# Performance work log

Measured on AMD Instinct MI355X. Metric: run time of the kernel, lower is better.

Reference implementation:

```python
import jax, jax.numpy as jnp
import numpy as np

IGNORE_INDEX = -100
BETA = 0.1
ALPHA = 1.0
LABEL_SMOOTHING = 0.0
GAMMA = 0.5

B, T, H, V = 8, 512, 2048, 32000


def setup_inputs() -> dict:
    key = jax.random.key(0)
    k1, k2, k3 = jax.random.split(key, 3)
    lin_weight = jax.random.normal(k1, (V, H), dtype=jnp.float32) * 0.02
    _input = jax.random.normal(k2, (B, T, H), dtype=jnp.float32)
    target = jax.random.randint(k3, (B, T), 0, V, dtype=jnp.int64)
    bias = jnp.zeros((V,), dtype=jnp.float32)
    return {"lin_weight": lin_weight, "_input": _input, "target": target, "bias": bias}


def reference(lin_weight, _input, target, bias):
    # Fused linear + SimPO preference loss (unfused jax reference).
    # _input: (B, T, H); first B/2 rows are 'chosen', last B/2 are 'rejected'.
    b = _input.shape[0]
    half = b // 2
    # logits: (B, T, V) -- the big tensor the Liger kernel avoids materializing
    logits = jnp.einsum("bth,vh->btv", _input, lin_weight) + bias
    log_probs = jax.nn.log_softmax(logits, axis=-1)
    # per-token log prob of the target token: (B, T)
    tok_logps = jnp.take_along_axis(log_probs, target[..., None], axis=-1)[..., 0]
    mask = (target != IGNORE_INDEX)
    maskf = mask.astype(tok_logps.dtype)
    # average log prob per sequence (SimPO length-normalization)
    avg_logps = (tok_logps * maskf).sum(-1) / maskf.sum(-1)
    chosen_logps = avg_logps[:half]
    rejected_logps = avg_logps[half:]
    # NLL loss on chosen half (compute_nll_loss=True), sum / num valid chosen tokens
    nll_loss = -(tok_logps[:half] * maskf[:half]).sum() / maskf[:half].sum()
    # SimPO sigmoid preference loss
    z = BETA * (chosen_logps - rejected_logps) - GAMMA
    pref_loss = (-jax.nn.log_sigmoid(z) * (1.0 - LABEL_SMOOTHING)
                 - jax.nn.log_sigmoid(-z) * LABEL_SMOOTHING).sum() / half
    loss = ALPHA * nll_loss + pref_loss
    return loss
```

## Files before the change

kernel.cpp:

```cpp
#include <hip/hip_runtime.h>
#include <hip/hip_bf16.h>


constexpr int Bb = 8, Tt = 512, Hh = 2048, Vv = 32000;
constexpr int Mrows = Bb * Tt;
constexpr int K4 = Hh / 4;
constexpr int BM = 128, BN = 128, BK = 64;
constexpr int NRT = Mrows / BM;
constexpr int NVT = Vv / BN;
constexpr int NVT2 = NVT * 2;
constexpr int NKS = Hh / BK;
constexpr int LDK = BK + 8;

typedef __attribute__((ext_vector_type(8))) short short8;
typedef __attribute__((ext_vector_type(4))) float f32x4;
typedef unsigned short ushort_t;

__device__ __forceinline__ unsigned pkbf2(float x, float y) {
  const unsigned ux = __builtin_bit_cast(unsigned, x);
  const unsigned uy = __builtin_bit_cast(unsigned, y);
  const unsigned rx = (ux + 0x7fffu + ((ux >> 16) & 1u)) >> 16;
  const unsigned ry = (uy + 0x7fffu + ((uy >> 16) & 1u)) >> 16;
  return (rx & 0xffffu) | (ry << 16);
}

__device__ __forceinline__ void gload16(const void* g, void* l) {
  __builtin_amdgcn_global_load_lds(
      (const __attribute__((address_space(1))) unsigned*)g,
      (__attribute__((address_space(3))) unsigned*)l, 16, 0, 0);
}

__global__ __launch_bounds__(256) void cvt_kernel(
    const float* __restrict__ src, unsigned* __restrict__ dst, int n4)
{
  const int stride = gridDim.x * 256;
  for (int i = blockIdx.x * 256 + threadIdx.x; i < n4; i += stride) {
    const float4 v = ((const float4*)src)[i];
    uint2 o;
    o.x = pkbf2(v.x, v.y);
    o.y = pkbf2(v.z, v.w);
    ((uint2*)dst)[i] = o;
  }
}

__device__ __forceinline__ void lse_epilogue(
    f32x4 (&acc)[4][4], const float* __restrict__ bias,
    float* __restrict__ pmax, float* __restrict__ psum,
    int rt, int vt, int wr, int wc, int lane)
{
  const int lane15 = lane & 15, q = lane >> 4;
  const int pcol = vt * 2 + (wc >> 6);
  float bj[4];
#pragma unroll
  for (int j = 0; j < 4; ++j) bj[j] = bias[vt * BN + wc + j * 16 + lane15];
#pragma unroll
  for (int i = 0; i < 4; ++i) {
#pragma unroll
    for (int r = 0; r < 4; ++r) {
      const float v0 = acc[i][0][r] + bj[0];
      const float v1 = acc[i][1][r] + bj[1];
      const float v2 = acc[i][2][r] + bj[2];
      const float v3 = acc[i][3][r] + bj[3];
      float mx = fmaxf(fmaxf(v0, v1), fmaxf(v2, v3));
#pragma unroll
      for (int m = 1; m < 16; m <<= 1) mx = fmaxf(mx, __shfl_xor(mx, m));
      float sm = __expf(v0 - mx) + __expf(v1 - mx) + __expf(v2 - mx) + __expf(v3 - mx);
#pragma unroll
      for (int m = 1; m < 16; m <<= 1) sm += __shfl_xor(sm, m);
      if (lane15 == 0) {
        const int grow = rt * BM + wr + i * 16 + q * 4 + r;
        pmax[(size_t)grow * NVT2 + pcol] = mx;
        psum[(size_t)grow * NVT2 + pcol] = sm;
      }
    }
  }
}

__global__ __launch_bounds__(256) void gemm_bf16(
    const ushort_t* __restrict__ Wb, const ushort_t* __restrict__ inpb,
    const float* __restrict__ bias,
    float* __restrict__ pmax, float* __restrict__ psum)
{
  __shared__ ushort_t At[BM][BK];
  __shared__ ushort_t Bt[BN][BK];

  const int tid = threadIdx.x;
  const int o  = (blockIdx.x & 7) * (NRT * NVT / 8) + (blockIdx.x >> 3);
  const int vt = o >> 5;
  const int rt = o & 31;

  const int lane = tid & 63;
  const int wv = tid >> 6;
  const int wr = (wv >> 1) * 64;
  const int wc = (wv & 1) * 64;

  const ushort_t* gA = inpb + (size_t)(rt * BM + wv * 32 + (lane >> 3)) * Hh + (lane & 7) * 8;
  const ushort_t* gB = Wb   + (size_t)(vt * BN + wv * 32 + (lane >> 3)) * Hh + (lane & 7) * 8;
  ushort_t* lA = &At[0][0] + wv * 2048 + lane * 8;
  ushort_t* lB = &Bt[0][0] + wv * 2048 + lane * 8;

  f32x4 acc[4][4];
#pragma unroll
  for (int i = 0; i < 4; ++i)
#pragma unroll
    for (int j = 0; j < 4; ++j) acc[i][j] = {0.f, 0.f, 0.f, 0.f};

  for (int ks = 0; ks < NKS; ++ks) {
#pragma unroll
    for (int c = 0; c < 4; ++c) {
      gload16(gA + (size_t)c * 8 * Hh + ks * BK, lA + c * 512);
      gload16(gB + (size_t)c * 8 * Hh + ks * BK, lB + c * 512);
    }
    __syncthreads();
#pragma unroll
    for (int kk = 0; kk < 2; ++kk) {
      const int kb = kk * 32 + (lane >> 4) * 8;
      const int rr = lane & 15;
      short8 a[4], b[4];
#pragma unroll
      for (int i = 0; i < 4; ++i) a[i] = *(const short8*)&At[wr + i * 16 + rr][kb];
#pragma unroll
      for (int j = 0; j < 4; ++j) b[j] = *(const short8*)&Bt[wc + j * 16 + rr][kb];
#pragma unroll
      for (int i = 0; i < 4; ++i)
#pragma unroll
        for (int j = 0; j < 4; ++j)
          acc[i][j] = __builtin_amdgcn_mfma_f32_16x16x32_bf16(a[i], b[j], acc[i][j], 0, 0, 0);
    }
    __syncthreads();
  }

  lse_epilogue(acc, bias, pmax, psum, rt, vt, wr, wc, lane);
}

__global__ __launch_bounds__(256) void gemm_partials(
    const float* __restrict__ W, const float* __restrict__ inp,
    const float* __restrict__ bias,
    float* __restrict__ pmax, float* __restrict__ psum)
{
  __shared__ ushort_t At[BM][LDK];
  __shared__ ushort_t Bt[BN][LDK];

  const int tid = threadIdx.x;
  const int o  = (blockIdx.x & 7) * (NRT * NVT / 8) + (blockIdx.x >> 3);
  const int vt = o >> 5;
  const int rt = o & 31;

  const int lane = tid & 63;
  const int wv = tid >> 6;
  const int wr = (wv >> 1) * 64;
  const int wc = (wv & 1) * 64;
  const int r0 = tid >> 4;
  const int c4 = tid & 15;

  const float4* Ag = (const float4*)inp + (size_t)(rt * BM) * K4;
  const float4* Bg = (const float4*)W  + (size_t)(vt * BN) * K4;

  float4 ar[8], br[8];
  auto issue = [&](int ks) {
    const int kb = ks * (BK / 4);
#pragma unroll
    for (int it = 0; it < 8; ++it) {
      ar[it] = Ag[(size_t)(r0 + it * 16) * K4 + kb + c4];
      br[it] = Bg[(size_t)(r0 + it * 16) * K4 + kb + c4];
    }
  };

  f32x4 acc[4][4];
#pragma unroll
  for (int i = 0; i < 4; ++i)
#pragma unroll
    for (int j = 0; j < 4; ++j) acc[i][j] = {0.f, 0.f, 0.f, 0.f};

  issue(0);
  for (int ks = 0; ks < NKS; ++ks) {
    __syncthreads();
#pragma unroll
    for (int it = 0; it < 8; ++it) {
      uint2 ua, ub;
      ua.x = pkbf2(ar[it].x, ar[it].y); ua.y = pkbf2(ar[it].z, ar[it].w);
      ub.x = pkbf2(br[it].x, br[it].y); ub.y = pkbf2(br[it].z, br[it].w);
      *(uint2*)&At[r0 + it * 16][c4 * 4] = ua;
      *(uint2*)&Bt[r0 + it * 16][c4 * 4] = ub;
    }
    __syncthreads();
    if (ks + 1 < NKS) issue(ks + 1);
#pragma unroll
    for (int kk = 0; kk < 2; ++kk) {
      const int kb = kk * 32 + (lane >> 4) * 8;
      const int rr = lane & 15;
      short8 a[4], b[4];
#pragma unroll
      for (int i = 0; i < 4; ++i) a[i] = *(const short8*)&At[wr + i * 16 + rr][kb];
#pragma unroll
      for (int j = 0; j < 4; ++j) b[j] = *(const short8*)&Bt[wc + j * 16 + rr][kb];
#pragma unroll
      for (int i = 0; i < 4; ++i)
#pragma unroll
        for (int j = 0; j < 4; ++j)
          acc[i][j] = __builtin_amdgcn_mfma_f32_16x16x32_bf16(a[i], b[j], acc[i][j], 0, 0, 0);
    }
  }

  lse_epilogue(acc, bias, pmax, psum, rt, vt, wr, wc, lane);
}

__global__ __launch_bounds__(256) void tgt_kernel(
    const float* __restrict__ inp, const float* __restrict__ W,
    const int* __restrict__ target, const float* __restrict__ bias,
    float* __restrict__ tl)
{
  const int row = blockIdx.x;
  int tgt = target[row];
  const int tgtc = tgt < 0 ? 0 : tgt;
  const float4* a = (const float4*)inp + (size_t)row * K4;
  const float4* w = (const float4*)W + (size_t)tgtc * K4;
  const int t = threadIdx.x;
  float s = 0.f;
  for (int i = t; i < K4; i += 256) {
    const float4 x = a[i], y = w[i];
    s += x.x * y.x + x.y * y.y + x.z * y.z + x.w * y.w;
  }
#pragma unroll
  for (int m = 1; m < 64; m <<= 1) s += __shfl_xor(s, m);
  __shared__ float red[4];
  if ((t & 63) == 0) red[t >> 6] = s;
  __syncthreads();
  if (t == 0) tl[row] = red[0] + red[1] + red[2] + red[3] + bias[tgtc];
}

__global__ __launch_bounds__(64) void lse_kernel(
    const float* __restrict__ pmax, const float* __restrict__ psum,
    const float* __restrict__ tl, float* __restrict__ tok)
{
  const int row = blockIdx.x;
  const int l = threadIdx.x;
  const float* pm = pmax + (size_t)row * NVT2;
  const float* ps = psum + (size_t)row * NVT2;
  float M = -3.4e38f;
  for (int t = l; t < NVT2; t += 64) M = fmaxf(M, pm[t]);
#pragma unroll
  for (int m = 1; m < 64; m <<= 1) M = fmaxf(M, __shfl_xor(M, m));
  float S = 0.f;
  for (int t = l; t < NVT2; t += 64) S += ps[t] * __expf(pm[t] - M);
#pragma unroll
  for (int m = 1; m < 64; m <<= 1) S += __shfl_xor(S, m);
  if (l == 0) tok[row] = tl[row] - (M + logf(S));
}

__global__ __launch_bounds__(512) void final_kernel(
    const float* __restrict__ tok, const int* __restrict__ target,
    float* __restrict__ out)
{
  const int w = threadIdx.x >> 6;
  const int l = threadIdx.x & 63;
  float s = 0.f, c = 0.f;
  for (int i = l; i < Tt; i += 64) {
    const int row = w * Tt + i;
    const bool msk = target[row] != -100;
    s += msk ? tok[row] : 0.f;
    c += msk ? 1.f : 0.f;
  }
#pragma unroll
  for (int m = 1; m < 64; m <<= 1) { s += __shfl_xor(s, m); c += __shfl_xor(c, m); }
  __shared__ float sums[8], cnts[8];
  if (l == 0) { sums[w] = s; cnts[w] = c; }
  __syncthreads();
  if (threadIdx.x == 0) {
    float avg[8];
    float nsum = 0.f, ncnt = 0.f;
    for (int b = 0; b < 8; ++b) {
      avg[b] = sums[b] / cnts[b];
      if (b < 4) { nsum += sums[b]; ncnt += cnts[b]; }
    }
    const float nll = -nsum / ncnt;
    float pref = 0.f;
    for (int i = 0; i < 4; ++i) {
      const float z = 0.1f * (avg[i] - avg[i + 4]) - 0.5f;
      const float ls = fminf(z, 0.f) - log1pf(__expf(-fabsf(z)));
      pref += -ls;
    }
    pref *= 0.25f;
    out[0] = 1.0f * nll + pref;
  }
}

extern "C" void kernel_launch(void* const* d_in, const int* in_sizes, int n_in,
                              void* d_out, int out_size, void* d_ws, size_t ws_size,
                              hipStream_t stream) {
  const float* W    = (const float*)d_in[0];
  const float* inp  = (const float*)d_in[1];
  const int*   tgt  = (const int*)d_in[2];
  const float* bias = (const float*)d_in[3];
  char* ws = (char*)d_ws;

  constexpr size_t szWb   = (size_t)Vv * Hh * 2;
  constexpr size_t szInb  = (size_t)Mrows * Hh * 2;
  constexpr size_t szPart = (size_t)Mrows * NVT2 * 4;
  constexpr size_t need   = szWb + szInb + 2 * szPart + 2 * (size_t)Mrows * 4;

  if (ws_size >= need) {
    ushort_t* Wb   = (ushort_t*)ws;
    ushort_t* inpb = (ushort_t*)(ws + szWb);
    float* pmax = (float*)(ws + szWb + szInb);
    float* psum = (float*)(ws + szWb + szInb + szPart);
    float* tl   = (float*)(ws + szWb + szInb + 2 * szPart);
    float* tok  = (float*)(ws + szWb + szInb + 2 * szPart + (size_t)Mrows * 4);

    hipLaunchKernelGGL(cvt_kernel, dim3(2048), dim3(256), 0, stream,
                       W, (unsigned*)Wb, Vv * Hh / 4);
    hipLaunchKernelGGL(cvt_kernel, dim3(2048), dim3(256), 0, stream,
                       inp, (unsigned*)inpb, Mrows * Hh / 4);
    hipLaunchKernelGGL(gemm_bf16, dim3(NRT * NVT), dim3(256), 0, stream,
                       Wb, inpb, bias, pmax, psum);
    hipLaunchKernelGGL(tgt_kernel, dim3(Mrows), dim3(256), 0, stream,
                       inp, W, tgt, bias, tl);
    hipLaunchKernelGGL(lse_kernel, dim3(Mrows), dim3(64), 0, stream,
                       pmax, psum, tl, tok);
    hipLaunchKernelGGL(final_kernel, dim3(1), dim3(512), 0, stream,
                       tok, tgt, (float*)d_out);
  } else {
    float* pmax = (float*)ws;
    float* psum = (float*)(ws + szPart);
    float* tl   = (float*)(ws + 2 * szPart);
    float* tok  = (float*)(ws + 2 * szPart + (size_t)Mrows * 4);

    hipLaunchKernelGGL(gemm_partials, dim3(NRT * NVT), dim3(256), 0, stream,
                       W, inp, bias, pmax, psum);
    hipLaunchKernelGGL(tgt_kernel, dim3(Mrows), dim3(256), 0, stream,
                       inp, W, tgt, bias, tl);
    hipLaunchKernelGGL(lse_kernel, dim3(Mrows), dim3(64), 0, stream,
                       pmax, psum, tl, tok);
    hipLaunchKernelGGL(final_kernel, dim3(1), dim3(512), 0, stream,
                       tok, tgt, (float*)d_out);
  }
}
```

Measured before the change: 1.135 ms.

## Replace bf16 GEMM with 256x256 tiled, double-buffered, swizzled LDS pipeline

```diff
diff --git a/kernel.cpp b/kernel.cpp
--- a/kernel.cpp
+++ b/kernel.cpp
@@ -5,12 +5,10 @@
 constexpr int Bb = 8, Tt = 512, Hh = 2048, Vv = 32000;
 constexpr int Mrows = Bb * Tt;
 constexpr int K4 = Hh / 4;
-constexpr int BM = 128, BN = 128, BK = 64;
-constexpr int NRT = Mrows / BM;
-constexpr int NVT = Vv / BN;
-constexpr int NVT2 = NVT * 2;
-constexpr int NKS = Hh / BK;
-constexpr int LDK = BK + 8;
+constexpr int NVT2 = Vv / 64;
+constexpr int NT64 = Hh / 64;
+constexpr int BMf = 128, BNf = 128, LDK = 64 + 8;
+constexpr int NRTf = Mrows / BMf, NVTf = Vv / BNf, NKSf = Hh / 64;
 
 typedef __attribute__((ext_vector_type(8))) short short8;
 typedef __attribute__((ext_vector_type(4))) float f32x4;
@@ -43,18 +41,128 @@
   }
 }
 
-__device__ __forceinline__ void lse_epilogue(
-    f32x4 (&acc)[4][4], const float* __restrict__ bias,
-    float* __restrict__ pmax, float* __restrict__ psum,
-    int rt, int vt, int wr, int wc, int lane)
-{
-  const int lane15 = lane & 15, q = lane >> 4;
-  const int pcol = vt * 2 + (wc >> 6);
+__global__ __launch_bounds__(512, 2) void gemm256(
+    const ushort_t* __restrict__ Wb, const ushort_t* __restrict__ inpb,
+    const float* __restrict__ bias,
+    float* __restrict__ pmax, float* __restrict__ psum)
+{
+  extern __shared__ ushort_t lds[];
+
+  const int tid = threadIdx.x;
+  const int l  = tid & 63;
+  const int wv = tid >> 6;
+  const int wm = wv >> 2;
+  const int wn = wv & 3;
+
+  const int o  = ((int)blockIdx.x & 7) * 250 + ((int)blockIdx.x >> 3);
+  const int bn = o >> 4;
+  const int bm = o & 15;
+  const int rowA0 = bm * 256, rowB0 = bn * 256;
+
+  const int segr = l >> 3;
+  const int csrc = (l & 7) ^ segr;
+  const int arow = l & 15;
+  const int kcb  = l >> 4;
+  const int sx   = l & 7;
+
+  auto stage = [&](int H) {
+    if (H >= 4 * NT64) return;
+    const int T = H >> 2, m = H & 3;
+    const ushort_t* src = (m < 2) ? inpb : Wb;
+    const int r0 = ((m < 2) ? rowA0 : rowB0) + (m & 1) * 128;
+    ushort_t* reg = lds + ((((T & 1) << 2) | m) << 13);
+    const int kc = T * 64 + csrc * 8;
+#pragma unroll
+    for (int s = 0; s < 2; ++s) {
+      const int seg = s * 8 + wv;
+      gload16(src + (size_t)(r0 + seg * 8 + segr) * Hh + kc,
+              reg + seg * 512 + l * 8);
+    }
+  };
+
+  f32x4 acc[8][4];
+#pragma unroll
+  for (int i = 0; i < 8; ++i)
+#pragma unroll
+    for (int j = 0; j < 4; ++j) acc[i][j] = {0.f, 0.f, 0.f, 0.f};
+
+#pragma unroll
+  for (int h = 0; h < 6; ++h) stage(h);
+  asm volatile("s_waitcnt vmcnt(4)" ::: "memory");
+  __builtin_amdgcn_s_barrier();
+
+  const int browbase = (wn & 1) * 64;
+  for (int t = 0; t < NT64; ++t) {
+    const int bA = ((((t & 1) << 2) | wm) << 13);
+    const int bB = ((((t & 1) << 2) | (2 + (wn >> 1))) << 13);
+    short8 a0[8], a1[8], b0[4], b1[4];
+
+#pragma unroll
+    for (int i = 0; i < 8; ++i)
+      a0[i] = *(const short8*)(lds + bA + (i * 16 + arow) * 64 + ((kcb ^ sx) * 8));
+#pragma unroll
+    for (int j = 0; j < 4; ++j)
+      b0[j] = *(const short8*)(lds + bB + (browbase + j * 16 + arow) * 64 + ((kcb ^ sx) * 8));
+    stage(4 * t + 6);
+    __builtin_amdgcn_s_barrier();
+    __builtin_amdgcn_s_setprio(1);
+#pragma unroll
+    for (int i = 0; i < 8; ++i)
+#pragma unroll
+      for (int j = 0; j < 2; ++j)
+        acc[i][j] = __builtin_amdgcn_mfma_f32_16x16x32_bf16(a0[i], b0[j], acc[i][j], 0, 0, 0);
+    __builtin_amdgcn_s_setprio(0);
+    __builtin_amdgcn_s_barrier();
+
+#pragma unroll
+    for (int i = 0; i < 8; ++i)
+      a1[i] = *(const short8*)(lds + bA + (i * 16 + arow) * 64 + (((4 + kcb) ^ sx) * 8));
+#pragma unroll
+    for (int j = 0; j < 4; ++j)
+      b1[j] = *(const short8*)(lds + bB + (browbase + j * 16 + arow) * 64 + (((4 + kcb) ^ sx) * 8));
+    stage(4 * t + 7);
+    __builtin_amdgcn_s_barrier();
+    __builtin_amdgcn_s_setprio(1);
+#pragma unroll
+    for (int i = 0; i < 8; ++i)
+#pragma unroll
+      for (int j = 2; j < 4; ++j)
+        acc[i][j] = __builtin_amdgcn_mfma_f32_16x16x32_bf16(a0[i], b0[j], acc[i][j], 0, 0, 0);
+    __builtin_amdgcn_s_setprio(0);
+    __builtin_amdgcn_s_barrier();
+
+    stage(4 * t + 8);
+    __builtin_amdgcn_s_barrier();
+    __builtin_amdgcn_s_setprio(1);
+#pragma unroll
+    for (int i = 0; i < 8; ++i)
+#pragma unroll
+      for (int j = 0; j < 2; ++j)
+        acc[i][j] = __builtin_amdgcn_mfma_f32_16x16x32_bf16(a1[i], b1[j], acc[i][j], 0, 0, 0);
+    __builtin_amdgcn_s_setprio(0);
+    __builtin_amdgcn_s_barrier();
+
+    stage(4 * t + 9);
+    __builtin_amdgcn_s_barrier();
+    __builtin_amdgcn_s_setprio(1);
+#pragma unroll
+    for (int i = 0; i < 8; ++i)
+#pragma unroll
+      for (int j = 2; j < 4; ++j)
+        acc[i][j] = __builtin_amdgcn_mfma_f32_16x16x32_bf16(a1[i], b1[j], acc[i][j], 0, 0, 0);
+    __builtin_amdgcn_s_setprio(0);
+    if (t < NT64 - 2)      asm volatile("s_waitcnt vmcnt(4)" ::: "memory");
+    else if (t == NT64 - 2) asm volatile("s_waitcnt vmcnt(0)" ::: "memory");
+    __builtin_amdgcn_s_barrier();
+  }
+
+  const int q = l >> 4;
+  const int pcol = bn * 4 + wn;
   float bj[4];
 #pragma unroll
-  for (int j = 0; j < 4; ++j) bj[j] = bias[vt * BN + wc + j * 16 + lane15];
-#pragma unroll
-  for (int i = 0; i < 4; ++i) {
+  for (int j = 0; j < 4; ++j) bj[j] = bias[bn * 256 + wn * 64 + j * 16 + arow];
+#pragma unroll
+  for (int i = 0; i < 8; ++i) {
 #pragma unroll
     for (int r = 0; r < 4; ++r) {
       const float v0 = acc[i][0][r] + bj[0];
@@ -67,70 +175,13 @@
       float sm = __expf(v0 - mx) + __expf(v1 - mx) + __expf(v2 - mx) + __expf(v3 - mx);
 #pragma unroll
       for (int m = 1; m < 16; m <<= 1) sm += __shfl_xor(sm, m);
-      if (lane15 == 0) {
-        const int grow = rt * BM + wr + i * 16 + q * 4 + r;
+      if (arow == 0) {
+        const int grow = bm * 256 + wm * 128 + i * 16 + q * 4 + r;
         pmax[(size_t)grow * NVT2 + pcol] = mx;
         psum[(size_t)grow * NVT2 + pcol] = sm;
       }
     }
   }
-}
-
-__global__ __launch_bounds__(256) void gemm_bf16(
-    const ushort_t* __restrict__ Wb, const ushort_t* __restrict__ inpb,
-    const float* __restrict__ bias,
-    float* __restrict__ pmax, float* __restrict__ psum)
-{
-  __shared__ ushort_t At[BM][BK];
-  __shared__ ushort_t Bt[BN][BK];
-
-  const int tid = threadIdx.x;
-  const int o  = (blockIdx.x & 7) * (NRT * NVT / 8) + (blockIdx.x >> 3);
-  const int vt = o >> 5;
-  const int rt = o & 31;
-
-  const int lane = tid & 63;
-  const int wv = tid >> 6;
-  const int wr = (wv >> 1) * 64;
-  const int wc = (wv & 1) * 64;
-
-  const ushort_t* gA = inpb + (size_t)(rt * BM + wv * 32 + (lane >> 3)) * Hh + (lane & 7) * 8;
-  const ushort_t* gB = Wb   + (size_t)(vt * BN + wv * 32 + (lane >> 3)) * Hh + (lane & 7) * 8;
-  ushort_t* lA = &At[0][0] + wv * 2048 + lane * 8;
-  ushort_t* lB = &Bt[0][0] + wv * 2048 + lane * 8;
-
-  f32x4 acc[4][4];
-#pragma unroll
-  for (int i = 0; i < 4; ++i)
-#pragma unroll
-    for (int j = 0; j < 4; ++j) acc[i][j] = {0.f, 0.f, 0.f, 0.f};
-
-  for (int ks = 0; ks < NKS; ++ks) {
-#pragma unroll
-    for (int c = 0; c < 4; ++c) {
-      gload16(gA + (size_t)c * 8 * Hh + ks * BK, lA + c * 512);
-      gload16(gB + (size_t)c * 8 * Hh + ks * BK, lB + c * 512);
-    }
-    __syncthreads();
-#pragma unroll
-    for (int kk = 0; kk < 2; ++kk) {
-      const int kb = kk * 32 + (lane >> 4) * 8;
-      const int rr = lane & 15;
-      short8 a[4], b[4];
-#pragma unroll
-      for (int i = 0; i < 4; ++i) a[i] = *(const short8*)&At[wr + i * 16 + rr][kb];
-#pragma unroll
-      for (int j = 0; j < 4; ++j) b[j] = *(const short8*)&Bt[wc + j * 16 + rr][kb];
-#pragma unroll
-      for (int i = 0; i < 4; ++i)
-#pragma unroll
-        for (int j = 0; j < 4; ++j)
-          acc[i][j] = __builtin_amdgcn_mfma_f32_16x16x32_bf16(a[i], b[j], acc[i][j], 0, 0, 0);
-    }
-    __syncthreads();
-  }
-
-  lse_epilogue(acc, bias, pmax, psum, rt, vt, wr, wc, lane);
 }
 
 __global__ __launch_bounds__(256) void gemm_partials(
@@ -138,11 +189,11 @@
     const float* __restrict__ bias,
     float* __restrict__ pmax, float* __restrict__ psum)
 {
-  __shared__ ushort_t At[BM][LDK];
-  __shared__ ushort_t Bt[BN][LDK];
+  __shared__ ushort_t At[BMf][LDK];
+  __shared__ ushort_t Bt[BNf][LDK];
 
   const int tid = threadIdx.x;
-  const int o  = (blockIdx.x & 7) * (NRT * NVT / 8) + (blockIdx.x >> 3);
+  const int o  = (blockIdx.x & 7) * (NRTf * NVTf / 8) + (blockIdx.x >> 3);
   const int vt = o >> 5;
   const int rt = o & 31;
 
@@ -153,12 +204,12 @@
   const int r0 = tid >> 4;
   const int c4 = tid & 15;
 
-  const float4* Ag = (const float4*)inp + (size_t)(rt * BM) * K4;
-  const float4* Bg = (const float4*)W  + (size_t)(vt * BN) * K4;
+  const float4* Ag = (const float4*)inp + (size_t)(rt * BMf) * K4;
+  const float4* Bg = (const float4*)W  + (size_t)(vt * BNf) * K4;
 
   float4 ar[8], br[8];
   auto issue = [&](int ks) {
-    const int kb = ks * (BK / 4);
+    const int kb = ks * 16;
 #pragma unroll
     for (int it = 0; it < 8; ++it) {
       ar[it] = Ag[(size_t)(r0 + it * 16) * K4 + kb + c4];
@@ -173,7 +224,7 @@
     for (int j = 0; j < 4; ++j) acc[i][j] = {0.f, 0.f, 0.f, 0.f};
 
   issue(0);
-  for (int ks = 0; ks < NKS; ++ks) {
+  for (int ks = 0; ks < NKSf; ++ks) {
     __syncthreads();
 #pragma unroll
     for (int it = 0; it < 8; ++it) {
@@ -184,7 +235,7 @@
       *(uint2*)&Bt[r0 + it * 16][c4 * 4] = ub;
     }
     __syncthreads();
-    if (ks + 1 < NKS) issue(ks + 1);
+    if (ks + 1 < NKSf) issue(ks + 1);
 #pragma unroll
     for (int kk = 0; kk < 2; ++kk) {
       const int kb = kk * 32 + (lane >> 4) * 8;
@@ -202,7 +253,32 @@
     }
   }
 
-  lse_epilogue(acc, bias, pmax, psum, rt, vt, wr, wc, lane);
+  const int lane15 = lane & 15, q = lane >> 4;
+  const int pcol = vt * 2 + (wc >> 6);
+  float bj[4];
+#pragma unroll
+  for (int j = 0; j < 4; ++j) bj[j] = bias[vt * BNf + wc + j * 16 + lane15];
+#pragma unroll
+  for (int i = 0; i < 4; ++i) {
+#pragma unroll
+    for (int r = 0; r < 4; ++r) {
+      const float v0 = acc[i][0][r] + bj[0];
+      const float v1 = acc[i][1][r] + bj[1];
+      const float v2 = acc[i][2][r] + bj[2];
+      const float v3 = acc[i][3][r] + bj[3];
+      float mx = fmaxf(fmaxf(v0, v1), fmaxf(v2, v3));
+#pragma unroll
+      for (int m = 1; m < 16; m <<= 1) mx = fmaxf(mx, __shfl_xor(mx, m));
+      float sm = __expf(v0 - mx) + __expf(v1 - mx) + __expf(v2 - mx) + __expf(v3 - mx);
+#pragma unroll
+      for (int m = 1; m < 16; m <<= 1) sm += __shfl_xor(sm, m);
+      if (lane15 == 0) {
+        const int grow = rt * BMf + wr + i * 16 + q * 4 + r;
+        pmax[(size_t)grow * NVT2 + pcol] = mx;
+        psum[(size_t)grow * NVT2 + pcol] = sm;
+      }
+    }
+  }
 }
 
 __global__ __launch_bounds__(256) void tgt_kernel(
@@ -311,7 +387,7 @@
                        W, (unsigned*)Wb, Vv * Hh / 4);
     hipLaunchKernelGGL(cvt_kernel, dim3(2048), dim3(256), 0, stream,
                        inp, (unsigned*)inpb, Mrows * Hh / 4);
-    hipLaunchKernelGGL(gemm_bf16, dim3(NRT * NVT), dim3(256), 0, stream,
+    hipLaunchKernelGGL(gemm256, dim3(2000), dim3(512), 131072, stream,
                        Wb, inpb, bias, pmax, psum);
     hipLaunchKernelGGL(tgt_kernel, dim3(Mrows), dim3(256), 0, stream,
                        inp, W, tgt, bias, tl);
@@ -325,7 +401,7 @@
     float* tl   = (float*)(ws + 2 * szPart);
     float* tok  = (float*)(ws + 2 * szPart + (size_t)Mrows * 4);
 
-    hipLaunchKernelGGL(gemm_partials, dim3(NRT * NVT), dim3(256), 0, stream,
+    hipLaunchKernelGGL(gemm_partials, dim3(NRTf * NVTf), dim3(256), 0, stream,
                        W, inp, bias, pmax, psum);
     hipLaunchKernelGGL(tgt_kernel, dim3(Mrows), dim3(256), 0, stream,
                        inp, W, tgt, bias, tl);
```

Result: faster. 922.9 us (-18.7%).
